# Optimization experiments

Measured on AMD Instinct MI355X. Metric: run time of the kernel, lower is better.

The kernel has to match this reference:

```python
import jax, jax.numpy as jnp
import numpy as np

N = 200000   # nodes
E = 600000   # edges
D = 128      # emb_dim
L = 5        # num_layer
G = 2000     # graphs in batch
T = 1        # num_tasks
NUM_ATOM_TYPE = 120
NUM_CHIRALITY = 3
NUM_BOND_TYPE = 6
NUM_BOND_DIR = 3
EPS = 1e-5


def setup_inputs() -> dict:
    key = jax.random.key(0)
    ks = jax.random.split(key, 16)
    s = lambda k, shape, fan: jax.random.normal(k, shape, jnp.float32) * (1.0 / np.sqrt(fan))
    return {
        "x_idx": jax.random.randint(ks[0], (N, 2), 0, 3),
        "edge_index": jax.random.randint(ks[1], (2, E), 0, N),
        "edge_attr": jax.random.randint(ks[2], (E, 2), 0, 3),
        "batch": jnp.sort(jax.random.randint(ks[3], (N,), 0, G)),
        "atom_emb1": s(ks[4], (NUM_ATOM_TYPE, D), D),
        "atom_emb2": s(ks[5], (NUM_CHIRALITY, D), D),
        "edge_emb1": s(ks[6], (L, NUM_BOND_TYPE, D), D),
        "edge_emb2": s(ks[7], (L, NUM_BOND_DIR, D), D),
        "W1": s(ks[8], (L, D, 2 * D), D),
        "b1": jnp.zeros((L, 2 * D), jnp.float32),
        "W2": s(ks[9], (L, 2 * D, D), 2 * D),
        "b2": jnp.zeros((L, D), jnp.float32),
        "bn_gamma": jnp.ones((L, D), jnp.float32),
        "bn_beta": jnp.zeros((L, D), jnp.float32),
        "Wp": s(ks[10], (D, T), D),
        "bp": jnp.zeros((T,), jnp.float32),
    }


def reference(atom_emb1, atom_emb2, edge_emb1, edge_emb2, W1, b1, W2, b2,
              bn_gamma, bn_beta, Wp, bp, x_idx, edge_index, edge_attr, batch):
    # node input embedding: sum of atom-type and chirality embeddings
    h = atom_emb1[x_idx[:, 0]] + atom_emb2[x_idx[:, 1]]  # [N, D]
    src, dst = edge_index[0], edge_index[1]
    ea0, ea1 = edge_attr[:, 0], edge_attr[:, 1]
    for l in range(L):
        # GINConv: edge embedding + neighbor add-aggregation (incl. self loop, bond type 4 / dir 0)
        e = edge_emb1[l][ea0] + edge_emb2[l][ea1]                 # [E, D]
        msg = h[src] + e                                          # gather + fuse
        agg = jax.ops.segment_sum(msg, dst, num_segments=N)       # scatter-add
        agg = agg + h + (edge_emb1[l][4] + edge_emb2[l][0])       # self-loop message
        # GIN MLP: Linear(D,2D) -> ReLU -> Linear(2D,D)
        z = jnp.maximum(agg @ W1[l] + b1[l], 0.0) @ W2[l] + b2[l]
        # BatchNorm1d over nodes (training-mode batch statistics)
        mu = z.mean(0)
        var = z.var(0)
        z = (z - mu) * jax.lax.rsqrt(var + EPS) * bn_gamma[l] + bn_beta[l]
        # ReLU except after the last layer; dropout ratio is 0 (identity)
        h = jnp.maximum(z, 0.0) if l < L - 1 else z
    # JK 'last' node representation -> sum pooling over graphs -> task head
    pooled = jax.ops.segment_sum(h, batch, num_segments=G)        # [G, D]
    return pooled @ Wp + bp                                       # [G, T]
```

## Files before the change

kernel.cpp:

```cpp
#include <hip/hip_runtime.h>

typedef unsigned int uint;
typedef unsigned short ushort;
typedef _Float16 f16_t;
typedef f16_t f16x8 __attribute__((ext_vector_type(8)));
typedef ushort ushort8 __attribute__((ext_vector_type(8)));
typedef float f32x4 __attribute__((ext_vector_type(4)));

#define NN 200000
#define EE 600000
#define LL 5
#define GG 2000
#define SCAN_NB 782

__device__ __forceinline__ ushort f2h(float f) {
  f16_t h = (f16_t)f;
  return __builtin_bit_cast(ushort, h);
}
__device__ __forceinline__ float h2f(ushort u) {
  return (float)__builtin_bit_cast(f16_t, u);
}
__device__ __forceinline__ float hlo(uint u) { return h2f((ushort)(u & 0xFFFFu)); }
__device__ __forceinline__ float hhi(uint u) { return h2f((ushort)(u >> 16)); }
__device__ __forceinline__ f16x8 ld8h(const uint4* p, int idx) {
  uint4 u = p[idx];
  return __builtin_bit_cast(f16x8, u);
}
__device__ __forceinline__ f16x8 bnrelu8(f16x8 u, f16x8 sc, f16x8 sh) {
  f16x8 r = u * sc + sh;
#pragma unroll
  for (int j = 0; j < 8; ++j) r[j] = r[j] > (f16_t)0.f ? r[j] : (f16_t)0.f;
  return r;
}

__global__ void k_setup(const float* __restrict__ W1, const float* __restrict__ W2,
                        ushort* __restrict__ w1s, ushort* __restrict__ w2s,
                        const float* __restrict__ ee1, const float* __restrict__ ee2,
                        const float* __restrict__ at1, const float* __restrict__ at2,
                        ushort* __restrict__ tabh, const int* __restrict__ xidx,
                        int* __restrict__ xcode, float* __restrict__ out,
                        const float* __restrict__ bp) {
  int i = blockIdx.x * 256 + threadIdx.x;
  if (i < 40960) {
    int lane = i & 63;
    int f = i >> 6;
    bool isW2 = false;
    if (f >= 320) { f -= 320; isW2 = true; }
    int l = f >> 6, rem = f & 63;
    ushort8 o;
    if (!isW2) {
      int kt = rem >> 4, nt = rem & 15;
      int n = nt * 16 + (lane & 15);
      int kbase = kt * 32 + (lane >> 4) * 8;
#pragma unroll
      for (int j = 0; j < 8; ++j) o[j] = f2h(W1[l * 32768 + (kbase + j) * 256 + n]);
      *(ushort8*)(w1s + f * 512 + lane * 8) = o;
    } else {
      int kt = rem >> 3, nt = rem & 7;
      int n = nt * 16 + (lane & 15);
      int kbase = kt * 32 + (lane >> 4) * 8;
#pragma unroll
      for (int j = 0; j < 8; ++j) o[j] = f2h(W2[l * 32768 + (kbase + j) * 128 + n]);
      *(ushort8*)(w2s + f * 512 + lane * 8) = o;
    }
  }
  if (i < 5760) {
    int l = i / 1152, rem = i % 1152;
    int ab = rem >> 7, c = rem & 127;
    int a = ab / 3, b = ab - a * 3;
    tabh[i] = f2h(ee1[(l * 6 + a) * 128 + c] + ee2[(l * 3 + b) * 128 + c]);
  } else if (i < 6400) {
    int j = i - 5760;
    int l = j >> 7, c = j & 127;
    tabh[i] = f2h(ee1[(l * 6 + 4) * 128 + c] + ee2[(l * 3 + 0) * 128 + c]);
  } else if (i < 7552) {
    int j = i - 6400;
    int ab = j >> 7, c = j & 127;
    int a = ab / 3, b = ab - a * 3;
    tabh[i] = f2h(at1[a * 128 + c] + at2[b * 128 + c]);
  }
  if (i < NN) xcode[i] = xidx[2 * i] * 3 + xidx[2 * i + 1];
  if (i < GG) out[i] = bp[0];
}

__global__ void k_count(const int* __restrict__ ei, int* __restrict__ counts) {
  int e = blockIdx.x * 256 + threadIdx.x;
  if (e < EE) atomicAdd(&counts[ei[EE + e]], 1);
}

__global__ void k_scanA(const int* __restrict__ counts, int* __restrict__ rowptr,
                        int* __restrict__ bsums) {
  __shared__ int sd[256];
  int tid = threadIdx.x;
  int g = blockIdx.x * 256 + tid;
  int v = (g < NN) ? counts[g] : 0;
  sd[tid] = v;
  __syncthreads();
  for (int o = 1; o < 256; o <<= 1) {
    int t = (tid >= o) ? sd[tid - o] : 0;
    __syncthreads();
    sd[tid] += t;
    __syncthreads();
  }
  if (g < NN) rowptr[g] = sd[tid] - v;
  if (tid == 255) bsums[blockIdx.x] = sd[tid];
}

__global__ void k_scanB(int* __restrict__ bsums) {
  __shared__ int sd[1024];
  int tid = threadIdx.x;
  int v = (tid < SCAN_NB) ? bsums[tid] : 0;
  sd[tid] = v;
  __syncthreads();
  for (int o = 1; o < 1024; o <<= 1) {
    int t = (tid >= o) ? sd[tid - o] : 0;
    __syncthreads();
    sd[tid] += t;
    __syncthreads();
  }
  if (tid < SCAN_NB) bsums[tid] = sd[tid] - v;
}

__global__ void k_scanC(int* __restrict__ rowptr, const int* __restrict__ bsums) {
  int g = blockIdx.x * 256 + threadIdx.x;
  if (g < NN) rowptr[g] += bsums[blockIdx.x];
  if (g == 0) rowptr[NN] = EE;
}

__global__ void k_fill(const int* __restrict__ ei, const int* __restrict__ ea,
                       const int* __restrict__ xcode, int* __restrict__ cursor,
                       int* __restrict__ eslot) {
  int e = blockIdx.x * 256 + threadIdx.x;
  if (e < EE) {
    int dst = ei[EE + e];
    int src = ei[e];
    int a9 = ea[2 * e] * 3 + ea[2 * e + 1];
    int sc = xcode[src];
    int pos = atomicAdd(&cursor[dst], 1);
    eslot[pos] = src | (a9 << 18) | (sc << 22);
  }
}

__global__ void k_hist2(const int* __restrict__ rowptr, int* __restrict__ bhist) {
  __shared__ int h[256];
  int tid = threadIdx.x;
  h[tid] = 0;
  __syncthreads();
  int n = blockIdx.x * 256 + tid;
  if (n < NN) {
    int d = rowptr[n + 1] - rowptr[n];
    if (d > 255) d = 255;
    atomicAdd(&h[255 - d], 1);
  }
  __syncthreads();
  bhist[tid * SCAN_NB + blockIdx.x] = h[tid];
}

__global__ void k_hscanA(int* __restrict__ data, int* __restrict__ bsums) {
  __shared__ int sd[256];
  int tid = threadIdx.x;
  int g = blockIdx.x * 256 + tid;
  int v = data[g];
  sd[tid] = v;
  __syncthreads();
  for (int o = 1; o < 256; o <<= 1) {
    int t = (tid >= o) ? sd[tid - o] : 0;
    __syncthreads();
    sd[tid] += t;
    __syncthreads();
  }
  data[g] = sd[tid] - v;
  if (tid == 255) bsums[blockIdx.x] = sd[tid];
}

__global__ void k_hscanC(int* __restrict__ data, const int* __restrict__ bsums) {
  int g = blockIdx.x * 256 + threadIdx.x;
  data[g] += bsums[blockIdx.x];
}

__global__ void k_dfill2(const int* __restrict__ rowptr, const int* __restrict__ xcode,
                         const int* __restrict__ bpos, int4* __restrict__ ndesc) {
  __shared__ int h[256];
  int tid = threadIdx.x;
  h[tid] = 0;
  __syncthreads();
  int n = blockIdx.x * 256 + tid;
  if (n < NN) {
    int s = rowptr[n], e = rowptr[n + 1];
    int d = e - s;
    if (d > 255) d = 255;
    int r = atomicAdd(&h[255 - d], 1);
    int pos = bpos[(255 - d) * SCAN_NB + blockIdx.x] + r;
    ndesc[pos] = make_int4(n, s, e, xcode[n]);
  }
}

__global__ __launch_bounds__(256, 8) void k_layer(
    const ushort* __restrict__ zin, ushort* __restrict__ zout,
    const int4* __restrict__ ndesc, const ushort* __restrict__ tabh,
    const float* __restrict__ stats_in, const float* __restrict__ gamma,
    const float* __restrict__ beta,
    const int* __restrict__ eslot,
    const ushort* __restrict__ w1s, const ushort* __restrict__ w2s,
    const float* __restrict__ b1, const float* __restrict__ b2,
    float* __restrict__ stats, int layer) {
  __shared__ __align__(16) ushort BUF[32 * 264];
  __shared__ int4 ND[32];
  __shared__ float SS[256];
  __shared__ float BNP[256];
  ushort* AGG = BUF;
  ushort* T1 = BUF;
  ushort* ldsZ = BUF;
  const int tid = threadIdx.x;
  const int w = tid >> 6, lane = tid & 63;
  const int ln16 = lane & 15, sub = lane >> 4;
  const int row0 = blockIdx.x * 32;

  if (tid < 32) ND[tid] = ndesc[row0 + tid];
  if (layer > 0) {
    const float* sb = stats_in + (size_t)(layer - 1) * 16 * 256;
    float a = 0.f;
#pragma unroll
    for (int cp = 0; cp < 16; ++cp) a += sb[cp * 256 + tid];
    SS[tid] = a;
    __syncthreads();
    if (tid < 128) {
      float mu = SS[tid] * (1.0f / NN);
      float var = SS[128 + tid] * (1.0f / NN) - mu * mu;
      float sc = gamma[(layer - 1) * 128 + tid] * rsqrtf(var + 1e-5f);
      BNP[tid] = sc;
      BNP[128 + tid] = beta[(layer - 1) * 128 + tid] - mu * sc;
    }
  }
  __syncthreads();

  const uint4* combH = (const uint4*)(tabh + (size_t)layer * 1152);
  const uint4* atomH = (const uint4*)(tabh + 6400);
  const uint4* selfH = (const uint4*)(tabh + 5760 + layer * 128);
  const uint4* h4 = (const uint4*)zin;
  f16x8 sf = ld8h(selfH, ln16);
  f16x8 scv = {}, shv = {};
  if (layer > 0) {
#pragma unroll
    for (int j = 0; j < 8; ++j) {
      scv[j] = (f16_t)BNP[ln16 * 8 + j];
      shv[j] = (f16_t)BNP[128 + ln16 * 8 + j];
    }
  }

#pragma unroll
  for (int grp = 0; grp < 2; ++grp) {
    const int4 nd = ND[w * 8 + grp * 4 + sub];
    const int n = nd.x;
    const int s = nd.y, e = nd.z;
    f16x8 acc;
    if (layer == 0) {
      acc = ld8h(atomH, nd.w * 16 + ln16) + sf;
    } else {
      acc = bnrelu8(ld8h(h4, (size_t)n * 16 + ln16), scv, shv) + sf;
    }
    for (int base = s; base < e; base += 16) {
      int m = e - base;
      if (m > 16) m = 16;
      int slot = (ln16 < m) ? eslot[base + ln16] : 0;
      int jfull = m & ~3;
      int j = 0;
      for (; j < jfull; j += 4) {
        int sl0 = __shfl(slot, sub * 16 + j + 0, 64);
        int sl1 = __shfl(slot, sub * 16 + j + 1, 64);
        int sl2 = __shfl(slot, sub * 16 + j + 2, 64);
        int sl3 = __shfl(slot, sub * 16 + j + 3, 64);
        f16x8 p0, p1, p2, p3;
        if (layer == 0) {
          p0 = ld8h(atomH, ((sl0 >> 22) & 15) * 16 + ln16);
          p1 = ld8h(atomH, ((sl1 >> 22) & 15) * 16 + ln16);
          p2 = ld8h(atomH, ((sl2 >> 22) & 15) * 16 + ln16);
          p3 = ld8h(atomH, ((sl3 >> 22) & 15) * 16 + ln16);
        } else {
          p0 = ld8h(h4, (size_t)(sl0 & 0x3FFFF) * 16 + ln16);
          p1 = ld8h(h4, (size_t)(sl1 & 0x3FFFF) * 16 + ln16);
          p2 = ld8h(h4, (size_t)(sl2 & 0x3FFFF) * 16 + ln16);
          p3 = ld8h(h4, (size_t)(sl3 & 0x3FFFF) * 16 + ln16);
        }
        f16x8 c0 = ld8h(combH, ((sl0 >> 18) & 15) * 16 + ln16);
        f16x8 c1 = ld8h(combH, ((sl1 >> 18) & 15) * 16 + ln16);
        f16x8 c2 = ld8h(combH, ((sl2 >> 18) & 15) * 16 + ln16);
        f16x8 c3 = ld8h(combH, ((sl3 >> 18) & 15) * 16 + ln16);
        if (layer != 0) {
          p0 = bnrelu8(p0, scv, shv);
          p1 = bnrelu8(p1, scv, shv);
          p2 = bnrelu8(p2, scv, shv);
          p3 = bnrelu8(p3, scv, shv);
        }
        acc += p0 + c0;
        acc += p1 + c1;
        acc += p2 + c2;
        acc += p3 + c3;
      }
      for (; j < m; ++j) {
        int sl = __shfl(slot, sub * 16 + j, 64);
        f16x8 p0;
        if (layer == 0) {
          p0 = ld8h(atomH, ((sl >> 22) & 15) * 16 + ln16);
        } else {
          p0 = bnrelu8(ld8h(h4, (size_t)(sl & 0x3FFFF) * 16 + ln16), scv, shv);
        }
        f16x8 c0 = ld8h(combH, ((sl >> 18) & 15) * 16 + ln16);
        acc += p0 + c0;
      }
    }
    *(uint4*)&AGG[(w * 8 + grp * 4 + sub) * 136 + ln16 * 8] =
        __builtin_bit_cast(uint4, acc);
  }
  __syncthreads();

  const int lm = ln16, q = sub;
  f32x4 acc[2][4] = {};
  const ushort* w1b = w1s + layer * 64 * 512;
#pragma unroll
  for (int kt = 0; kt < 4; ++kt) {
    f16x8 af[2];
#pragma unroll
    for (int mt = 0; mt < 2; ++mt) {
      const ushort* p = AGG + (mt * 16 + lm) * 136 + kt * 32 + q * 8;
      af[mt] = __builtin_bit_cast(f16x8, *(const ushort8*)p);
    }
#pragma unroll
    for (int np = 0; np < 2; ++np) {
      f16x8 bf[2];
#pragma unroll
      for (int ni = 0; ni < 2; ++ni) {
        const ushort* p = w1b + (kt * 16 + w * 4 + np * 2 + ni) * 512 + lane * 8;
        bf[ni] = __builtin_bit_cast(f16x8, *(const ushort8*)p);
      }
#pragma unroll
      for (int mt = 0; mt < 2; ++mt)
#pragma unroll
        for (int ni = 0; ni < 2; ++ni)
          acc[mt][np * 2 + ni] = __builtin_amdgcn_mfma_f32_16x16x32_f16(
              af[mt], bf[ni], acc[mt][np * 2 + ni], 0, 0, 0);
    }
  }
  __syncthreads();
#pragma unroll
  for (int nt = 0; nt < 4; ++nt) {
    int n = w * 64 + nt * 16 + lm;
    float bias = b1[layer * 256 + n];
#pragma unroll
    for (int mt = 0; mt < 2; ++mt)
#pragma unroll
      for (int r = 0; r < 4; ++r) {
        float v = fmaxf(acc[mt][nt][r] + bias, 0.0f);
        T1[(mt * 16 + q * 4 + r) * 264 + n] = f2h(v);
      }
  }
  __syncthreads();

  f32x4 acc2[2][2] = {};
  const ushort* w2b = w2s + layer * 64 * 512;
#pragma unroll
  for (int kt = 0; kt < 8; ++kt) {
    f16x8 af[2], bf[2];
#pragma unroll
    for (int mt = 0; mt < 2; ++mt) {
      const ushort* p = T1 + (mt * 16 + lm) * 264 + kt * 32 + q * 8;
      af[mt] = __builtin_bit_cast(f16x8, *(const ushort8*)p);
    }
#pragma unroll
    for (int nt = 0; nt < 2; ++nt) {
      const ushort* p = w2b + (kt * 8 + w * 2 + nt) * 512 + lane * 8;
      bf[nt] = __builtin_bit_cast(f16x8, *(const ushort8*)p);
    }
#pragma unroll
    for (int mt = 0; mt < 2; ++mt)
#pragma unroll
      for (int nt = 0; nt < 2; ++nt)
        acc2[mt][nt] = __builtin_amdgcn_mfma_f32_16x16x32_f16(af[mt], bf[nt], acc2[mt][nt], 0, 0, 0);
  }
  __syncthreads();
  float ssum[2], ssq[2];
#pragma unroll
  for (int nt = 0; nt < 2; ++nt) {
    int n = w * 32 + nt * 16 + lm;
    float bias = b2[layer * 128 + n];
    ssum[nt] = 0.f;
    ssq[nt] = 0.f;
#pragma unroll
    for (int mt = 0; mt < 2; ++mt)
#pragma unroll
      for (int r = 0; r < 4; ++r) {
        float v = acc2[mt][nt][r] + bias;
        ldsZ[(mt * 16 + q * 4 + r) * 136 + n] = f2h(v);
        ssum[nt] += v;
        ssq[nt] += v * v;
      }
    ssum[nt] += __shfl_xor(ssum[nt], 16, 64);
    ssum[nt] += __shfl_xor(ssum[nt], 32, 64);
    ssq[nt] += __shfl_xor(ssq[nt], 16, 64);
    ssq[nt] += __shfl_xor(ssq[nt], 32, 64);
  }
  if (lane < 16) {
    int cp = blockIdx.x & 15;
    float* sb = stats + (size_t)(layer * 16 + cp) * 256;
#pragma unroll
    for (int nt = 0; nt < 2; ++nt) {
      int col = w * 32 + nt * 16 + lane;
      atomicAdd(&sb[col], ssum[nt]);
      atomicAdd(&sb[128 + col], ssq[nt]);
    }
  }
  __syncthreads();
  uint* zo = (uint*)zout;
  for (int i = tid; i < 32 * 64; i += 256) {
    int row = i >> 6, cpx = i & 63;
    uint v = *(const uint*)&ldsZ[row * 136 + cpx * 2];
    zo[(size_t)ND[row].x * 64 + cpx] = v;
  }
}

__global__ __launch_bounds__(256) void k_pool(const ushort* __restrict__ z,
                                              const float* __restrict__ stats,
                                              const float* __restrict__ gamma,
                                              const float* __restrict__ beta,
                                              const int* __restrict__ batch,
                                              const float* __restrict__ Wp,
                                              float* __restrict__ out) {
  __shared__ float SS[256];
  __shared__ float BNP[256];
  const int tid = threadIdx.x;
  const int w = tid >> 6, lane = tid & 63;
  const int nb = blockIdx.x * 64 + w * 16;
  {
    const float* sb = stats + (size_t)4 * 16 * 256;
    float a = 0.f;
#pragma unroll
    for (int cp = 0; cp < 16; ++cp) a += sb[cp * 256 + tid];
    SS[tid] = a;
    __syncthreads();
    if (tid < 128) {
      float mu = SS[tid] * (1.0f / NN);
      float var = SS[128 + tid] * (1.0f / NN) - mu * mu;
      float sc = gamma[4 * 128 + tid] * rsqrtf(var + 1e-5f);
      BNP[tid] = sc;
      BNP[128 + tid] = beta[4 * 128 + tid] - mu * sc;
    }
    __syncthreads();
  }
  float2 wp = ((const float2*)Wp)[lane];
  float2 scv = make_float2(BNP[2 * lane], BNP[2 * lane + 1]);
  float2 shv = make_float2(BNP[128 + 2 * lane], BNP[128 + 2 * lane + 1]);
  const uint* z32 = (const uint*)z;
  int bb = (lane < 16) ? batch[nb + lane] : 0;
  int curb = __shfl(bb, 0);
  float run = 0.f;
#pragma unroll
  for (int i = 0; i < 16; ++i) {
    int b = __shfl(bb, i);
    uint u = z32[(size_t)(nb + i) * 64 + lane];
    float dot = fmaf(hlo(u), scv.x, shv.x) * wp.x + fmaf(hhi(u), scv.y, shv.y) * wp.y;
#pragma unroll
    for (int off = 32; off > 0; off >>= 1) dot += __shfl_xor(dot, off, 64);
    if (b != curb) {
      if (lane == 0) atomicAdd(&out[curb], run);
      run = 0.f;
      curb = b;
    }
    run += dot;
  }
  if (lane == 0) atomicAdd(&out[curb], run);
}

extern "C" void kernel_launch(void* const* d_in, const int* in_sizes, int n_in,
                              void* d_out, int out_size, void* d_ws, size_t ws_size,
                              hipStream_t stream) {
  (void)in_sizes; (void)n_in; (void)out_size; (void)ws_size;
  const int* xidx = (const int*)d_in[0];
  const int* eidx = (const int*)d_in[1];
  const int* eattr = (const int*)d_in[2];
  const int* batch = (const int*)d_in[3];
  const float* at1 = (const float*)d_in[4];
  const float* at2 = (const float*)d_in[5];
  const float* ee1 = (const float*)d_in[6];
  const float* ee2 = (const float*)d_in[7];
  const float* W1 = (const float*)d_in[8];
  const float* b1 = (const float*)d_in[9];
  const float* W2 = (const float*)d_in[10];
  const float* b2 = (const float*)d_in[11];
  const float* gamma = (const float*)d_in[12];
  const float* beta = (const float*)d_in[13];
  const float* Wp = (const float*)d_in[14];
  const float* bp = (const float*)d_in[15];
  float* out = (float*)d_out;

  char* ws = (char*)d_ws;
  size_t off = 0;
  auto alloc = [&](size_t bytes) -> void* {
    void* p = ws + off;
    off = (off + bytes + 255) & ~(size_t)255;
    return p;
  };
  ushort* bufA = (ushort*)alloc((size_t)NN * 128 * 2);
  ushort* bufB = (ushort*)alloc((size_t)NN * 128 * 2);
  ushort* w1s = (ushort*)alloc(320 * 512 * 2);
  ushort* w2s = (ushort*)alloc(320 * 512 * 2);
  int* rowptr = (int*)alloc((NN + 1) * 4);
  int* cursor = (int*)alloc((size_t)NN * 4);
  int* eslot = (int*)alloc((size_t)EE * 4);
  int* bsums = (int*)alloc(1024 * 4);
  ushort* tabh = (ushort*)alloc(7552 * 2);
  int* xcode = (int*)alloc((size_t)NN * 4);
  float* stats = (float*)alloc((size_t)LL * 16 * 256 * 4);
  int* bhist = (int*)alloc((size_t)SCAN_NB * 256 * 4);
  int* bsums2 = (int*)alloc(1024 * 4);
  int4* ndesc = (int4*)alloc((size_t)NN * 16);

  hipMemsetAsync(cursor, 0, (size_t)NN * 4, stream);
  hipMemsetAsync(stats, 0, (size_t)LL * 16 * 256 * 4, stream);
  k_setup<<<SCAN_NB, 256, 0, stream>>>(W1, W2, w1s, w2s, ee1, ee2, at1, at2, tabh, xidx,
                                       xcode, out, bp);
  k_count<<<(EE + 255) / 256, 256, 0, stream>>>(eidx, cursor);
  k_scanA<<<SCAN_NB, 256, 0, stream>>>(cursor, rowptr, bsums);
  k_scanB<<<1, 1024, 0, stream>>>(bsums);
  k_scanC<<<SCAN_NB, 256, 0, stream>>>(rowptr, bsums);
  hipMemcpyAsync(cursor, rowptr, (size_t)NN * 4, hipMemcpyDeviceToDevice, stream);
  k_fill<<<(EE + 255) / 256, 256, 0, stream>>>(eidx, eattr, xcode, cursor, eslot);
  k_hist2<<<SCAN_NB, 256, 0, stream>>>(rowptr, bhist);
  k_hscanA<<<SCAN_NB, 256, 0, stream>>>(bhist, bsums2);
  k_scanB<<<1, 1024, 0, stream>>>(bsums2);
  k_hscanC<<<SCAN_NB, 256, 0, stream>>>(bhist, bsums2);
  k_dfill2<<<SCAN_NB, 256, 0, stream>>>(rowptr, xcode, bhist, ndesc);

  for (int l = 0; l < LL; ++l) {
    ushort* zo = (l & 1) ? bufB : bufA;
    const ushort* zi = (l & 1) ? bufA : bufB;
    k_layer<<<NN / 32, 256, 0, stream>>>((l == 0) ? bufA : zi, zo, ndesc, tabh, stats,
                                         gamma, beta, eslot, w1s, w2s, b1, b2,
                                         stats, l);
  }
  k_pool<<<NN / 64, 256, 0, stream>>>(bufA, stats, gamma, beta, batch, Wp, out);
}
```

Measured before the change: 548.4 us.

## Double rows per block in layer kernel to 64 with 512 threads

The fused GIN layer kernel now handles 64 node rows per block with 8 waves instead of 32 rows with 4 waves. The MLP tiling changes so each wave computes all 64 rows against a narrower column slice. Each weight fragment loaded from global memory is therefore reused across four row tiles instead of two, and half as many blocks issue stats atomics. In exchange LDS use per block doubles and the launch bound drops to 6, which may lower occupancy. The unseen aggregation section has to index correctly for the 8 waves, which cannot be checked here.

```diff
diff --git a/kernel.cpp b/kernel.cpp
--- a/kernel.cpp
+++ b/kernel.cpp
@@ -195,7 +195,7 @@
   }
 }
 
-__global__ __launch_bounds__(256, 8) void k_layer(
+__global__ __launch_bounds__(512, 6) void k_layer(
     const ushort* __restrict__ zin, ushort* __restrict__ zout,
     const int4* __restrict__ ndesc, const ushort* __restrict__ tabh,
     const float* __restrict__ stats_in, const float* __restrict__ gamma,
@@ -204,8 +204,8 @@
     const ushort* __restrict__ w1s, const ushort* __restrict__ w2s,
     const float* __restrict__ b1, const float* __restrict__ b2,
     float* __restrict__ stats, int layer) {
-  __shared__ __align__(16) ushort BUF[32 * 264];
-  __shared__ int4 ND[32];
+  __shared__ __align__(16) ushort BUF[64 * 264];
+  __shared__ int4 ND[64];
   __shared__ float SS[256];
   __shared__ float BNP[256];
   ushort* AGG = BUF;
@@ -214,15 +214,17 @@
   const int tid = threadIdx.x;
   const int w = tid >> 6, lane = tid & 63;
   const int ln16 = lane & 15, sub = lane >> 4;
-  const int row0 = blockIdx.x * 32;
-
-  if (tid < 32) ND[tid] = ndesc[row0 + tid];
+  const int row0 = blockIdx.x * 64;
+
+  if (tid < 64) ND[tid] = ndesc[row0 + tid];
   if (layer > 0) {
-    const float* sb = stats_in + (size_t)(layer - 1) * 16 * 256;
-    float a = 0.f;
-#pragma unroll
-    for (int cp = 0; cp < 16; ++cp) a += sb[cp * 256 + tid];
-    SS[tid] = a;
+    if (tid < 256) {
+      const float* sb = stats_in + (size_t)(layer - 1) * 16 * 256;
+      float a = 0.f;
+#pragma unroll
+      for (int cp = 0; cp < 16; ++cp) a += sb[cp * 256 + tid];
+      SS[tid] = a;
+    }
     __syncthreads();
     if (tid < 128) {
       float mu = SS[tid] * (1.0f / NN);
@@ -315,39 +317,36 @@
   __syncthreads();
 
   const int lm = ln16, q = sub;
-  f32x4 acc[2][4] = {};
+  f32x4 acc[4][2] = {};
   const ushort* w1b = w1s + layer * 64 * 512;
 #pragma unroll
   for (int kt = 0; kt < 4; ++kt) {
-    f16x8 af[2];
-#pragma unroll
-    for (int mt = 0; mt < 2; ++mt) {
+    f16x8 af[4];
+#pragma unroll
+    for (int mt = 0; mt < 4; ++mt) {
       const ushort* p = AGG + (mt * 16 + lm) * 136 + kt * 32 + q * 8;
       af[mt] = __builtin_bit_cast(f16x8, *(const ushort8*)p);
     }
-#pragma unroll
-    for (int np = 0; np < 2; ++np) {
-      f16x8 bf[2];
-#pragma unroll
-      for (int ni = 0; ni < 2; ++ni) {
-        const ushort* p = w1b + (kt * 16 + w * 4 + np * 2 + ni) * 512 + lane * 8;
-        bf[ni] = __builtin_bit_cast(f16x8, *(const ushort8*)p);
-      }
-#pragma unroll
-      for (int mt = 0; mt < 2; ++mt)
-#pragma unroll
-        for (int ni = 0; ni < 2; ++ni)
-          acc[mt][np * 2 + ni] = __builtin_amdgcn_mfma_f32_16x16x32_f16(
-              af[mt], bf[ni], acc[mt][np * 2 + ni], 0, 0, 0);
-    }
-  }
-  __syncthreads();
-#pragma unroll
-  for (int nt = 0; nt < 4; ++nt) {
-    int n = w * 64 + nt * 16 + lm;
+    f16x8 bf[2];
+#pragma unroll
+    for (int ni = 0; ni < 2; ++ni) {
+      const ushort* p = w1b + (kt * 16 + w * 2 + ni) * 512 + lane * 8;
+      bf[ni] = __builtin_bit_cast(f16x8, *(const ushort8*)p);
+    }
+#pragma unroll
+    for (int mt = 0; mt < 4; ++mt)
+#pragma unroll
+      for (int ni = 0; ni < 2; ++ni)
+        acc[mt][ni] = __builtin_amdgcn_mfma_f32_16x16x32_f16(
+            af[mt], bf[ni], acc[mt][ni], 0, 0, 0);
+  }
+  __syncthreads();
+#pragma unroll
+  for (int nt = 0; nt < 2; ++nt) {
+    int n = w * 32 + nt * 16 + lm;
     float bias = b1[layer * 256 + n];
 #pragma unroll
-    for (int mt = 0; mt < 2; ++mt)
+    for (int mt = 0; mt < 4; ++mt)
 #pragma unroll
       for (int r = 0; r < 4; ++r) {
         float v = fmaxf(acc[mt][nt][r] + bias, 0.0f);
@@ -356,62 +355,53 @@
   }
   __syncthreads();
 
-  f32x4 acc2[2][2] = {};
+  f32x4 acc2[4] = {};
   const ushort* w2b = w2s + layer * 64 * 512;
 #pragma unroll
   for (int kt = 0; kt < 8; ++kt) {
-    f16x8 af[2], bf[2];
-#pragma unroll
-    for (int mt = 0; mt < 2; ++mt) {
+    f16x8 af[4], bf;
+#pragma unroll
+    for (int mt = 0; mt < 4; ++mt) {
       const ushort* p = T1 + (mt * 16 + lm) * 264 + kt * 32 + q * 8;
       af[mt] = __builtin_bit_cast(f16x8, *(const ushort8*)p);
     }
-#pragma unroll
-    for (int nt = 0; nt < 2; ++nt) {
-      const ushort* p = w2b + (kt * 8 + w * 2 + nt) * 512 + lane * 8;
-      bf[nt] = __builtin_bit_cast(f16x8, *(const ushort8*)p);
-    }
-#pragma unroll
-    for (int mt = 0; mt < 2; ++mt)
-#pragma unroll
-      for (int nt = 0; nt < 2; ++nt)
-        acc2[mt][nt] = __builtin_amdgcn_mfma_f32_16x16x32_f16(af[mt], bf[nt], acc2[mt][nt], 0, 0, 0);
-  }
-  __syncthreads();
-  float ssum[2], ssq[2];
-#pragma unroll
-  for (int nt = 0; nt < 2; ++nt) {
-    int n = w * 32 + nt * 16 + lm;
+    {
+      const ushort* p = w2b + (kt * 8 + w) * 512 + lane * 8;
+      bf = __builtin_bit_cast(f16x8, *(const ushort8*)p);
+    }
+#pragma unroll
+    for (int mt = 0; mt < 4; ++mt)
+      acc2[mt] = __builtin_amdgcn_mfma_f32_16x16x32_f16(af[mt], bf, acc2[mt], 0, 0, 0);
+  }
+  __syncthreads();
+  float ssum = 0.f, ssq = 0.f;
+  {
+    int n = w * 16 + lm;
     float bias = b2[layer * 128 + n];
-    ssum[nt] = 0.f;
-    ssq[nt] = 0.f;
-#pragma unroll
-    for (int mt = 0; mt < 2; ++mt)
+#pragma unroll
+    for (int mt = 0; mt < 4; ++mt)
 #pragma unroll
       for (int r = 0; r < 4; ++r) {
-        float v = acc2[mt][nt][r] + bias;
+        float v = acc2[mt][r] + bias;
         ldsZ[(mt * 16 + q * 4 + r) * 136 + n] = f2h(v);
-        ssum[nt] += v;
-        ssq[nt] += v * v;
+        ssum += v;
+        ssq += v * v;
       }
-    ssum[nt] += __shfl_xor(ssum[nt], 16, 64);
-    ssum[nt] += __shfl_xor(ssum[nt], 32, 64);
-    ssq[nt] += __shfl_xor(ssq[nt], 16, 64);
-    ssq[nt] += __shfl_xor(ssq[nt], 32, 64);
+    ssum += __shfl_xor(ssum, 16, 64);
+    ssum += __shfl_xor(ssum, 32, 64);
+    ssq += __shfl_xor(ssq, 16, 64);
+    ssq += __shfl_xor(ssq, 32, 64);
   }
   if (lane < 16) {
     int cp = blockIdx.x & 15;
     float* sb = stats + (size_t)(layer * 16 + cp) * 256;
-#pragma unroll
-    for (int nt = 0; nt < 2; ++nt) {
-      int col = w * 32 + nt * 16 + lane;
-      atomicAdd(&sb[col], ssum[nt]);
-      atomicAdd(&sb[128 + col], ssq[nt]);
-    }
+    int col = w * 16 + lane;
+    atomicAdd(&sb[col], ssum);
+    atomicAdd(&sb[128 + col], ssq);
   }
   __syncthreads();
   uint* zo = (uint*)zout;
-  for (int i = tid; i < 32 * 64; i += 256) {
+  for (int i = tid; i < 64 * 64; i += 512) {
     int row = i >> 6, cpx = i & 63;
     uint v = *(const uint*)&ldsZ[row * 136 + cpx * 2];
     zo[(size_t)ND[row].x * 64 + cpx] = v;
@@ -533,7 +523,7 @@
   for (int l = 0; l < LL; ++l) {
     ushort* zo = (l & 1) ? bufB : bufA;
     const ushort* zi = (l & 1) ? bufA : bufB;
-    k_layer<<<NN / 32, 256, 0, stream>>>((l == 0) ? bufA : zi, zo, ndesc, tabh, stats,
+    k_layer<<<NN / 64, 512, 0, stream>>>((l == 0) ? bufA : zi, zo, ndesc, tabh, stats,
                                          gamma, beta, eslot, w1s, w2s, b1, b2,
                                          stats, l);
   }
```

Measured after the change: 519.1 us. -5.3%, faster.
